# Optimization experiments

Measured on AMD Instinct MI355X. Metric: run time of the kernel, lower is better.

The kernel has to match this reference:

```python
import jax, jax.numpy as jnp
import numpy as np

SLOPE = 25.0  # fast_sigmoid surrogate slope
THR = 1.0     # snntorch Leaky default threshold

@jax.custom_vjp
def spike(x):
    # heaviside forward, fast-sigmoid surrogate backward
    return (x > 0).astype(x.dtype)

def _spike_fwd(x):
    return spike(x), x

def _spike_bwd(x, g):
    return (g / (SLOPE * jnp.abs(x) + 1.0) ** 2,)

spike.defvjp(_spike_fwd, _spike_bwd)


def _xavier(k, shape):
    fan_out, fan_in = shape
    lim = np.sqrt(6.0 / (fan_in + fan_out)).astype(np.float32)
    return jax.random.uniform(k, shape, jnp.float32, -lim, lim)


def setup_inputs() -> dict:
    key = jax.random.key(0)
    ks = jax.random.split(key, 6)
    B, T, NI, H1, H2, NO = 256, 100, 512, 1024, 1024, 10
    return {
        "x": jax.random.normal(ks[0], (B, T, NI), jnp.float32),
        "W1": _xavier(ks[1], (H1, NI)),
        "W1r": _xavier(ks[2], (H1, H1)),
        "W2": _xavier(ks[3], (H2, H1)),
        "W2r": _xavier(ks[4], (H2, H2)),
        "Wout": _xavier(ks[5], (NO, H2)),
        "beta1": jnp.float32(0.9),
        "beta2": jnp.float32(0.9),
        "beta_out": jnp.float32(0.9),
    }


def reference(x, W1, W1r, W2, W2r, Wout, beta1, beta2, beta_out):
    B, T, NI = x.shape
    H1, H2, NO = W1.shape[0], W2.shape[0], Wout.shape[0]
    b1 = jnp.clip(beta1, 0.0, 1.0)
    b2 = jnp.clip(beta2, 0.0, 1.0)
    bo = jnp.clip(beta_out, 0.0, 1.0)
    xt = jnp.transpose(x, (1, 0, 2))  # [T, B, NI]

    def step(carry, x_t):
        mem1, spk1, mem2, spk2, mem_out = carry
        # layer 1: feedforward + recurrent current, leaky integrate, subtract-reset
        cur1 = x_t @ W1.T + spk1 @ W1r.T
        reset1 = jax.lax.stop_gradient((mem1 > THR).astype(mem1.dtype))
        mem1 = b1 * mem1 + cur1 - reset1 * THR
        spk1 = spike(mem1 - THR)
        # layer 2
        cur2 = spk1 @ W2.T + spk2 @ W2r.T
        reset2 = jax.lax.stop_gradient((mem2 > THR).astype(mem2.dtype))
        mem2 = b2 * mem2 + cur2 - reset2 * THR
        spk2 = spike(mem2 - THR)
        # readout: reset_mechanism='none'
        mem_out = bo * mem_out + spk2 @ Wout.T
        return (mem1, spk1, mem2, spk2, mem_out), (spk1, mem_out)

    z = lambda n: jnp.zeros((B, n), x.dtype)
    carry0 = (z(H1), z(H1), z(H2), z(H2), z(NO))
    _, (spk1_rec, mem_out_rec) = jax.lax.scan(step, carry0, xt)
    return spk1_rec, mem_out_rec  # [T,B,H1], [T,B,NO]
```

## Files before the change

### kernel.cpp

```cpp
#include <hip/hip_runtime.h>

#define S_ELE (256 * 1024)
#define NBLK 1024
#define GRP  8
#define GSZ  (NBLK / GRP)

typedef float f32x4 __attribute__((ext_vector_type(4)));
typedef float f32x2 __attribute__((ext_vector_type(2)));

struct Ptrs {
    const float *x, *W1, *W1r, *W2, *W2r, *Wout;
    const float *b1, *b2, *bo;
    float *spk1_rec, *mout_rec;
    float *mem1, *mem2, *memo;
    float *w1rt, *w2t, *w2rt, *xw, *S2;
    unsigned *bar, *cnt1, *cnt2;
    unsigned short *idx1, *idx2;
    int t_ch;
};

__device__ __forceinline__ float clip01(float b) { return fminf(fmaxf(b, 0.0f), 1.0f); }
__device__ __forceinline__ float4 ld4(const float* p) { return *reinterpret_cast<const float4*>(p); }
__device__ __forceinline__ void   st4(float* p, float4 v) { *reinterpret_cast<float4*>(p) = v; }
__device__ __forceinline__ float2 ld2(const float* p) { return *reinterpret_cast<const float2*>(p); }
__device__ __forceinline__ void   st2(float* p, float2 v) { *reinterpret_cast<float2*>(p) = v; }
__device__ __forceinline__ void   st2nt(float* p, float2 v)
{
    f32x2 n = { v.x, v.y };
    __builtin_nontemporal_store(n, reinterpret_cast<f32x2*>(p));
}

__device__ __forceinline__ float4 memup(float4 mo, float4 cur, float b, float4* sv)
{
    float4 mn, s;
    mn.x = b * mo.x + cur.x - (mo.x > 1.0f ? 1.0f : 0.0f); s.x = (mn.x - 1.0f) > 0.0f ? 1.0f : 0.0f;
    mn.y = b * mo.y + cur.y - (mo.y > 1.0f ? 1.0f : 0.0f); s.y = (mn.y - 1.0f) > 0.0f ? 1.0f : 0.0f;
    mn.z = b * mo.z + cur.z - (mo.z > 1.0f ? 1.0f : 0.0f); s.z = (mn.z - 1.0f) > 0.0f ? 1.0f : 0.0f;
    mn.w = b * mo.w + cur.w - (mo.w > 1.0f ? 1.0f : 0.0f); s.w = (mn.w - 1.0f) > 0.0f ? 1.0f : 0.0f;
    *sv = s; return mn;
}
__device__ __forceinline__ float2 memup2(float2 mo, float2 cur, float b, float2* sv)
{
    float2 mn, s;
    mn.x = b * mo.x + cur.x - (mo.x > 1.0f ? 1.0f : 0.0f); s.x = (mn.x - 1.0f) > 0.0f ? 1.0f : 0.0f;
    mn.y = b * mo.y + cur.y - (mo.y > 1.0f ? 1.0f : 0.0f); s.y = (mn.y - 1.0f) > 0.0f ? 1.0f : 0.0f;
    *sv = s; return mn;
}

__device__ __forceinline__ void gbar(unsigned* bar)
{
    __syncthreads();
    if (threadIdx.x == 0) {
        unsigned g = __hip_atomic_load(&bar[0], __ATOMIC_RELAXED, __HIP_MEMORY_SCOPE_AGENT);
        unsigned* gc = &bar[8 + ((int)blockIdx.x & (GRP - 1)) * 32];
        unsigned a = __hip_atomic_fetch_add(gc, 1u, __ATOMIC_ACQ_REL, __HIP_MEMORY_SCOPE_AGENT);
        if (a == GSZ - 1) {
            __hip_atomic_store(gc, 0u, __ATOMIC_RELAXED, __HIP_MEMORY_SCOPE_AGENT);
            unsigned tp = __hip_atomic_fetch_add(&bar[1], 1u, __ATOMIC_ACQ_REL, __HIP_MEMORY_SCOPE_AGENT);
            if (tp == GRP - 1) {
                __hip_atomic_store(&bar[1], 0u, __ATOMIC_RELAXED, __HIP_MEMORY_SCOPE_AGENT);
                __hip_atomic_store(&bar[0], g + 1u, __ATOMIC_RELEASE, __HIP_MEMORY_SCOPE_AGENT);
            }
        }
        while (__hip_atomic_load(&bar[0], __ATOMIC_ACQUIRE, __HIP_MEMORY_SCOPE_AGENT) == g)
            __builtin_amdgcn_s_sleep(2);
    }
    __syncthreads();
}

__device__ __forceinline__ void tr32(float* sm, const float* src, float* dst, int tr, int tc)
{
    const int t = (int)threadIdx.x;
    const int r = t >> 3, c4 = (t & 7) << 2;
    __syncthreads();
    float4 v = ld4(src + (size_t)(tr * 32 + r) * 1024 + tc * 32 + c4);
    sm[r * 33 + c4 + 0] = v.x; sm[r * 33 + c4 + 1] = v.y;
    sm[r * 33 + c4 + 2] = v.z; sm[r * 33 + c4 + 3] = v.w;
    __syncthreads();
    const int kk = t >> 3, nn4 = (t & 7) << 2;
    float4 o;
    o.x = sm[(nn4 + 0) * 33 + kk]; o.y = sm[(nn4 + 1) * 33 + kk];
    o.z = sm[(nn4 + 2) * 33 + kk]; o.w = sm[(nn4 + 3) * 33 + kk];
    st4(dst + (size_t)(tc * 32 + kk) * 1024 + tr * 32 + nn4, o);
}

__device__ __forceinline__ void xw_tile(float* sm, const float* xA, const float* W1,
                                        float* out, int tm, int tn)
{
    float* As = sm;
    float* Bs = sm + 1056;
    const int t = (int)threadIdx.x;
    const int ar = t >> 1;
    const int ak = (t & 1) << 2;
    const int r0 = (t >> 4) << 3;
    const int c0 = (t & 15) << 3;
    const float* Ab = xA + (size_t)(tm * 128) * 51200;
    const float* Bb = W1 + (size_t)(tn * 128) * 512;
    float4 pa = ld4(Ab + (size_t)ar * 51200 + ak);
    float4 pb = ld4(Bb + (size_t)ar * 512 + ak);
    float acc[8][8] = {};
    for (int c = 0; c < 64; ++c) {
        __syncthreads();
        As[(ak + 0) * 132 + ar] = pa.x; As[(ak + 1) * 132 + ar] = pa.y;
        As[(ak + 2) * 132 + ar] = pa.z; As[(ak + 3) * 132 + ar] = pa.w;
        Bs[(ak + 0) * 132 + ar] = pb.x; Bs[(ak + 1) * 132 + ar] = pb.y;
        Bs[(ak + 2) * 132 + ar] = pb.z; Bs[(ak + 3) * 132 + ar] = pb.w;
        __syncthreads();
        if (c + 1 < 64) {
            const int ko = (c + 1) * 8;
            pa = ld4(Ab + (size_t)ar * 51200 + ko + ak);
            pb = ld4(Bb + (size_t)ar * 512 + ko + ak);
        }
        #pragma unroll
        for (int k = 0; k < 8; ++k) {
            float4 a0 = ld4(&As[k * 132 + r0]);
            float4 a1 = ld4(&As[k * 132 + r0 + 4]);
            float4 b0 = ld4(&Bs[k * 132 + c0]);
            float4 b1 = ld4(&Bs[k * 132 + c0 + 4]);
            float av[8] = {a0.x, a0.y, a0.z, a0.w, a1.x, a1.y, a1.z, a1.w};
            float bv[8] = {b0.x, b0.y, b0.z, b0.w, b1.x, b1.y, b1.z, b1.w};
            #pragma unroll
            for (int i = 0; i < 8; ++i)
                #pragma unroll
                for (int j = 0; j < 8; ++j)
                    acc[i][j] = fmaf(av[i], bv[j], acc[i][j]);
        }
    }
    #pragma unroll
    for (int i = 0; i < 8; ++i) {
        float* row = out + (size_t)(tm * 128 + r0 + i) * 1024 + tn * 128 + c0;
        st4(row,     make_float4(acc[i][0], acc[i][1], acc[i][2], acc[i][3]));
        st4(row + 4, make_float4(acc[i][4], acc[i][5], acc[i][6], acc[i][7]));
    }
}

template <int NC>
__device__ __forceinline__ void gatherN(const unsigned short* const lp[],
    const unsigned st[], const unsigned en[], const float* Wt, int n4, float4 c[])
{
    unsigned j[NC], e[NC];
    float4 pa[NC], pb[NC];
    #pragma unroll
    for (int q = 0; q < NC; ++q) {
        j[q] = st[q]; e[q] = en[q];
        c[q] = make_float4(0.f, 0.f, 0.f, 0.f);
        if (j[q] < e[q])     pa[q] = ld4(Wt + (size_t)lp[q][j[q]] * 1024 + n4);
        if (j[q] + 1 < e[q]) pb[q] = ld4(Wt + (size_t)lp[q][j[q] + 1] * 1024 + n4);
    }
    for (;;) {
        bool any = false;
        #pragma unroll
        for (int q = 0; q < NC; ++q) {
            if (j[q] < e[q]) {
                float4 v = pa[q];
                pa[q] = pb[q];
                if (j[q] + 2 < e[q]) pb[q] = ld4(Wt + (size_t)lp[q][j[q] + 2] * 1024 + n4);
                c[q].x += v.x; c[q].y += v.y; c[q].z += v.z; c[q].w += v.w;
                ++j[q];
                any = any || (j[q] < e[q]);
            }
        }
        if (!any) break;
    }
}

__device__ __forceinline__ void gather8_2(const unsigned short* lst,
    const unsigned pos[9], const float* Wt, int col, float2 c[8])
{
    unsigned j[8], e[8];
    float2 pa[8], pb[8];
    #pragma unroll
    for (int q = 0; q < 8; ++q) {
        j[q] = pos[q]; e[q] = pos[q + 1];
        c[q] = make_float2(0.f, 0.f);
        if (j[q] < e[q])     pa[q] = ld2(Wt + (size_t)lst[j[q]] * 1024 + col);
        if (j[q] + 1 < e[q]) pb[q] = ld2(Wt + (size_t)lst[j[q] + 1] * 1024 + col);
    }
    for (;;) {
        bool any = false;
        #pragma unroll
        for (int q = 0; q < 8; ++q) {
            if (j[q] < e[q]) {
                float2 v = pa[q];
                pa[q] = pb[q];
                if (j[q] + 2 < e[q]) pb[q] = ld2(Wt + (size_t)lst[j[q] + 2] * 1024 + col);
                c[q].x += v.x; c[q].y += v.y;
                ++j[q];
                any = any || (j[q] < e[q]);
            }
        }
        if (!any) break;
    }
}

__device__ __forceinline__ void build_seg_full(const float* s_spk,
    unsigned short* gidx, unsigned* gcnt)
{
    const int l = (int)threadIdx.x;
    #pragma unroll
    for (int w = 0; w < 8; ++w) {
        unsigned wtot = 0;
        #pragma unroll
        for (int i = 0; i < 2; ++i) {
            const int grp = w * 2 + i;
            float s = s_spk[grp * 64 + l];
            unsigned long long m = __ballot(s != 0.0f);
            unsigned off = (unsigned)__popcll(m & ((1ull << l) - 1ull));
            if (s != 0.0f) gidx[w * 128 + wtot + off] = (unsigned short)(grp * 64 + l);
            wtot += (unsigned)__popcll(m);
        }
        if (l == 0) gcnt[w] = wtot;
    }
}

__device__ __forceinline__ void build_seg_half(const float* s_half, int h,
    unsigned short* gidx, unsigned* gcnt)
{
    const int l = (int)threadIdx.x;
    #pragma unroll
    for (int wl = 0; wl < 4; ++wl) {
        const int w = 4 * h + wl;
        unsigned wtot = 0;
        #pragma unroll
        for (int i = 0; i < 2; ++i) {
            const int grp = wl * 2 + i;
            float s = s_half[grp * 64 + l];
            unsigned long long m = __ballot(s != 0.0f);
            unsigned off = (unsigned)__popcll(m & ((1ull << l) - 1ull));
            if (s != 0.0f)
                gidx[w * 128 + wtot + off] = (unsigned short)(h * 512 + grp * 64 + l);
            wtot += (unsigned)__popcll(m);
        }
        if (l == 0) gcnt[w] = wtot;
    }
}

__device__ __forceinline__ void stage_list(unsigned short* sl,
    const unsigned short* gseg, const unsigned* cw, const unsigned pos[9])
{
    const int t = (int)threadIdx.x;
    #pragma unroll
    for (int w = 0; w < 8; ++w)
        for (unsigned i = t; i < cw[w]; i += 256)
            sl[pos[w] + i] = gseg[w * 128 + i];
}

__device__ __forceinline__ void l1_half(float* sm, const Ptrs& p, int r, int h, int tau)
{
    const int t = (int)threadIdx.x;
    const int lc = t * 2;
    const int col = h * 512 + lc;
    const int pp = 1 - (tau & 1);
    const unsigned* cw = p.cnt1 + ((size_t)pp * 256 + r) * 8;
    unsigned pos[9];
    pos[0] = 0;
    #pragma unroll
    for (int w = 0; w < 8; ++w) pos[w + 1] = pos[w] + cw[w];
    unsigned short* sl16 = (unsigned short*)(sm + 512);
    stage_list(sl16, p.idx1 + ((size_t)pp * 256 + r) * 1024, cw, pos);
    __syncthreads();

    float2 c[8];
    gather8_2(sl16, pos, p.w1rt, col, c);

    const size_t base = (size_t)r * 1024 + col;
    const int slot = tau % p.t_ch;
    float2 acc = ld2(p.xw + (size_t)slot * S_ELE + base);
    #pragma unroll
    for (int w = 0; w < 8; ++w) { acc.x += c[w].x; acc.y += c[w].y; }
    const float bb = clip01(*p.b1);
    float2 mo = ld2(p.mem1 + base);
    float2 sv; float2 mn = memup2(mo, acc, bb, &sv);
    st2(p.mem1 + base, mn);
    st2nt(p.spk1_rec + (size_t)tau * S_ELE + base, sv);
    sm[lc] = sv.x; sm[lc + 1] = sv.y;
    __syncthreads();
    if (t < 64) build_seg_half(sm, h, p.idx1 + ((size_t)(tau & 1) * 256 + r) * 1024,
                               p.cnt1 + ((size_t)(tau & 1) * 256 + r) * 8);
}

__device__ __forceinline__ void l2g2(float* sm, const Ptrs& p, int g, int fam, int step)
{
    const int t = (int)threadIdx.x, n4 = t << 2;
    const bool rsel = fam >= 2;
    const bool hi = fam & 1;
    const int par = rsel ? (1 - (step & 1)) : (step & 1);
    const unsigned* cbase = (rsel ? p.cnt2 : p.cnt1) + (size_t)par * 256 * 8;
    const unsigned short* ibase = (rsel ? p.idx2 : p.idx1) + (size_t)par * 256 * 1024;
    const float* W = rsel ? p.w2rt : p.w2t;

    const unsigned short* lp[2];
    unsigned st[2], en[2];
    #pragma unroll
    for (int q = 0; q < 2; ++q) {
        const int r = 2 * g + q;
        const unsigned* cw = cbase + (size_t)r * 8;
        unsigned pos[9];
        pos[0] = 0;
        #pragma unroll
        for (int w = 0; w < 8; ++w) pos[w + 1] = pos[w] + cw[w];
        unsigned short* sl = (unsigned short*)sm + 1024 * q;
        stage_list(sl, ibase + (size_t)r * 1024, cw, pos);
        lp[q] = sl;
        st[q] = hi ? pos[4] : 0;
        en[q] = hi ? pos[8] : pos[4];
    }
    __syncthreads();
    float4 c[2];
    gatherN<2>(lp, st, en, W, n4, c);
    #pragma unroll
    for (int q = 0; q < 2; ++q)
        st4(p.S2 + (size_t)fam * S_ELE + (size_t)(2 * g + q) * 1024 + n4, c[q]);
}

__device__ __forceinline__ void upd2_row(float* sm, const Ptrs& p, int r, int step)
{
    const int t = (int)threadIdx.x, n4 = t << 2;
    const size_t base = (size_t)r * 1024 + n4;
    float4 p0 = ld4(p.S2 + base);
    float4 p1 = ld4(p.S2 + (size_t)S_ELE + base);
    float4 p2 = ld4(p.S2 + (size_t)2 * S_ELE + base);
    float4 p3 = ld4(p.S2 + (size_t)3 * S_ELE + base);
    float4 cur;
    cur.x = (p0.x + p1.x) + (p2.x + p3.x);
    cur.y = (p0.y + p1.y) + (p2.y + p3.y);
    cur.z = (p0.z + p1.z) + (p2.z + p3.z);
    cur.w = (p0.w + p1.w) + (p2.w + p3.w);
    const float bb = clip01(*p.b2);
    float4 mo = ld4(p.mem2 + base);
    float4 sv; float4 mn = memup(mo, cur, bb, &sv);
    st4(p.mem2 + base, mn);
    sm[n4 + 0] = sv.x; sm[n4 + 1] = sv.y; sm[n4 + 2] = sv.z; sm[n4 + 3] = sv.w;
    __syncthreads();
    if (t < 64) build_seg_full(sm, p.idx2 + ((size_t)(step & 1) * 256 + r) * 1024,
                               p.cnt2 + ((size_t)(step & 1) * 256 + r) * 8);
    const int wave = t >> 6, lane = t & 63;
    const float bo = clip01(*p.bo);
    float v[16];
    #pragma unroll
    for (int i = 0; i < 16; ++i) v[i] = sm[lane + 64 * i];
    float* rec = p.mout_rec + (size_t)step * 2560;
    for (int o = wave; o < 10; o += 4) {
        float sum = 0.0f;
        #pragma unroll
        for (int i = 0; i < 16; ++i)
            sum = fmaf(v[i], p.Wout[o * 1024 + lane + 64 * i], sum);
        #pragma unroll
        for (int off = 32; off > 0; off >>= 1) sum += __shfl_down(sum, off);
        if (lane == 0) {
            const float m = bo * p.memo[r * 10 + o] + sum;
            p.memo[r * 10 + o] = m;
            __builtin_nontemporal_store(m, &rec[r * 10 + o]);
        }
    }
}

__global__ __launch_bounds__(256, 4) void snn_all(Ptrs p)
{
    __shared__ float sm[2176];
    const int bid = (int)blockIdx.x;
    const int x = bid & 7, g = bid >> 3;

    for (int task = bid; task < 3072; task += NBLK) {
        const float* src = task < 1024 ? p.W1r : (task < 2048 ? p.W2 : p.W2r);
        float* dst = task < 1024 ? p.w1rt : (task < 2048 ? p.w2t : p.w2rt);
        const int id = task & 1023;
        tr32(sm, src, dst, id >> 5, id & 31);
    }
    gbar(p.bar);

    for (int tau = 0; tau <= 100; ++tau) {
        if (tau < 100 && (tau % p.t_ch) == 0) {
            const int ntask = p.t_ch * 16;
            for (int task = bid; task < ntask; task += NBLK) {
                const int tp = task >> 4, tile = task & 15;
                xw_tile(sm, p.x + (size_t)(tau + tp) * 512, p.W1,
                        p.xw + (size_t)tp * S_ELE, tile >> 3, tile & 7);
            }
            gbar(p.bar);
        }
        if (x < 4) {
            if (tau < 100) {
                const int idx = x * 128 + g;
                l1_half(sm, p, idx >> 1, idx & 1, tau);
            }
        } else {
            if (tau >= 1) l2g2(sm, p, g, x - 4, tau - 1);
        }
        gbar(p.bar);
        if (bid < 256 && tau >= 1) upd2_row(sm, p, bid, tau - 1);
        gbar(p.bar);
    }
}

__global__ __launch_bounds__(256, 4) void fb_pre(Ptrs p)
{
    __shared__ float sm[2176];
    for (int task = blockIdx.x; task < 3072; task += gridDim.x) {
        const float* src = task < 1024 ? p.W1r : (task < 2048 ? p.W2 : p.W2r);
        float* dst = task < 1024 ? p.w1rt : (task < 2048 ? p.w2t : p.w2rt);
        const int id = task & 1023;
        tr32(sm, src, dst, id >> 5, id & 31);
    }
}

__global__ __launch_bounds__(256, 4) void fb_xw(Ptrs p, int t0)
{
    __shared__ float sm[2176];
    const int task = (int)blockIdx.x;
    const int tp = task >> 4, tile = task & 15;
    xw_tile(sm, p.x + (size_t)(t0 + tp) * 512, p.W1,
            p.xw + (size_t)tp * S_ELE, tile >> 3, tile & 7);
}

__global__ __launch_bounds__(256, 4) void fb_p1(Ptrs p, int tau)
{
    __shared__ float sm[2176];
    const int bid = (int)blockIdx.x;
    const int x = bid & 7, g = bid >> 3;
    if (x < 4) {
        if (tau < 100) {
            const int idx = x * 128 + g;
            l1_half(sm, p, idx >> 1, idx & 1, tau);
        }
    } else {
        if (tau >= 1) l2g2(sm, p, g, x - 4, tau - 1);
    }
}

__global__ __launch_bounds__(256, 4) void fb_p2(Ptrs p, int tau)
{
    __shared__ float sm[2176];
    if (tau >= 1) upd2_row(sm, p, (int)blockIdx.x, tau - 1);
}

extern "C" void kernel_launch(void* const* d_in, const int* in_sizes, int n_in,
                              void* d_out, int out_size, void* d_ws, size_t ws_size,
                              hipStream_t stream)
{
    Ptrs p;
    p.x    = (const float*)d_in[0];
    p.W1   = (const float*)d_in[1];
    p.W1r  = (const float*)d_in[2];
    p.W2   = (const float*)d_in[3];
    p.W2r  = (const float*)d_in[4];
    p.Wout = (const float*)d_in[5];
    p.b1   = (const float*)d_in[6];
    p.b2   = (const float*)d_in[7];
    p.bo   = (const float*)d_in[8];

    float* out = (float*)d_out;
    p.spk1_rec = out;
    p.mout_rec = out + (size_t)100 * S_ELE;

    float* w = (float*)d_ws;
    p.mem1 = w;  w += S_ELE;
    p.mem2 = w;  w += S_ELE;
    p.memo = w;  w += 2560;
    p.bar  = (unsigned*)w;  w += 512;
    p.cnt1 = (unsigned*)w;  w += 4096;
    p.cnt2 = (unsigned*)w;  w += 4096;
    p.idx1 = (unsigned short*)w;  w += 262144;
    p.idx2 = (unsigned short*)w;  w += 262144;
    p.w1rt = w;  w += 1048576;
    p.w2t  = w;  w += 1048576;
    p.w2rt = w;  w += 1048576;
    p.S2   = w;  w += 4 * S_ELE;
    p.xw   = w;

    const size_t used = (size_t)(w - (float*)d_ws) * sizeof(float);
    int t_ch = 1;
    const int cands[] = {100, 50, 25, 20, 10, 5, 4, 2, 1};
    for (int c : cands)
        if (used + (size_t)c * S_ELE * sizeof(float) <= ws_size) { t_ch = c; break; }
    p.t_ch = t_ch;

    (void)hipMemsetAsync(p.mem1, 0,
                   ((size_t)2 * S_ELE + 2560 + 512 + 8192) * sizeof(float), stream);

    int maxb = 0;
    hipError_t qerr = hipOccupancyMaxActiveBlocksPerMultiprocessor(
        &maxb, (const void*)snn_all, 256, 0);
    bool coop = (qerr == hipSuccess && maxb >= 4);

    if (coop) {
        void* args[] = { (void*)&p };
        if (hipLaunchCooperativeKernel((const void*)snn_all, dim3(NBLK), dim3(256),
                                       args, 0, stream) != hipSuccess)
            coop = false;
    }

    if (!coop) {
        hipLaunchKernelGGL(fb_pre, dim3(NBLK), dim3(256), 0, stream, p);
        for (int tau = 0; tau <= 100; ++tau) {
            if (tau < 100 && (tau % t_ch) == 0)
                hipLaunchKernelGGL(fb_xw, dim3(t_ch * 16), dim3(256), 0, stream, p, tau);
            hipLaunchKernelGGL(fb_p1, dim3(NBLK), dim3(256), 0, stream, p, tau);
            hipLaunchKernelGGL(fb_p2, dim3(256), dim3(256), 0, stream, p, tau);
        }
    }
}
```

Before: 4.024 ms.

## Double the persistent grid to 2048 blocks with finer per-block work

Doubles the cooperative grid from 1024 to 2048 blocks at 8 blocks per CU. Each layer-1 block now handles a quarter row with one column per thread instead of half a row with two. Each layer-2 gather block now handles one row instead of two. Shared memory is halved and the xw tile loop uses 4-wide k chunks so more blocks fit per CU, aiming to hide gather latency through occupancy. The cost is more participants in every grid barrier, scalar rather than vector loads in the gathers, and a cooperative launch that now needs an occupancy of 8 to run.

After: 13.17 ms. 227% more time.

```diff
diff --git a/kernel.cpp b/kernel.cpp
--- a/kernel.cpp
+++ b/kernel.cpp
@@ -1,12 +1,11 @@
 #include <hip/hip_runtime.h>
 
 #define S_ELE (256 * 1024)
-#define NBLK 1024
+#define NBLK 2048
 #define GRP  8
 #define GSZ  (NBLK / GRP)
 
 typedef float f32x4 __attribute__((ext_vector_type(4)));
-typedef float f32x2 __attribute__((ext_vector_type(2)));
 
 struct Ptrs {
     const float *x, *W1, *W1r, *W2, *W2r, *Wout;
@@ -22,13 +21,6 @@
 __device__ __forceinline__ float clip01(float b) { return fminf(fmaxf(b, 0.0f), 1.0f); }
 __device__ __forceinline__ float4 ld4(const float* p) { return *reinterpret_cast<const float4*>(p); }
 __device__ __forceinline__ void   st4(float* p, float4 v) { *reinterpret_cast<float4*>(p) = v; }
-__device__ __forceinline__ float2 ld2(const float* p) { return *reinterpret_cast<const float2*>(p); }
-__device__ __forceinline__ void   st2(float* p, float2 v) { *reinterpret_cast<float2*>(p) = v; }
-__device__ __forceinline__ void   st2nt(float* p, float2 v)
-{
-    f32x2 n = { v.x, v.y };
-    __builtin_nontemporal_store(n, reinterpret_cast<f32x2*>(p));
-}
 
 __device__ __forceinline__ float4 memup(float4 mo, float4 cur, float b, float4* sv)
 {
@@ -39,12 +31,11 @@
     mn.w = b * mo.w + cur.w - (mo.w > 1.0f ? 1.0f : 0.0f); s.w = (mn.w - 1.0f) > 0.0f ? 1.0f : 0.0f;
     *sv = s; return mn;
 }
-__device__ __forceinline__ float2 memup2(float2 mo, float2 cur, float b, float2* sv)
-{
-    float2 mn, s;
-    mn.x = b * mo.x + cur.x - (mo.x > 1.0f ? 1.0f : 0.0f); s.x = (mn.x - 1.0f) > 0.0f ? 1.0f : 0.0f;
-    mn.y = b * mo.y + cur.y - (mo.y > 1.0f ? 1.0f : 0.0f); s.y = (mn.y - 1.0f) > 0.0f ? 1.0f : 0.0f;
-    *sv = s; return mn;
+__device__ __forceinline__ float memup1(float mo, float cur, float b, float* sv)
+{
+    float mn = b * mo + cur - (mo > 1.0f ? 1.0f : 0.0f);
+    *sv = (mn - 1.0f) > 0.0f ? 1.0f : 0.0f;
+    return mn;
 }
 
 __device__ __forceinline__ void gbar(unsigned* bar)
@@ -88,31 +79,27 @@
                                         float* out, int tm, int tn)
 {
     float* As = sm;
-    float* Bs = sm + 1056;
+    float* Bs = sm + 528;
     const int t = (int)threadIdx.x;
-    const int ar = t >> 1;
-    const int ak = (t & 1) << 2;
+    const int half = t >> 7;
+    const int row  = t & 127;
     const int r0 = (t >> 4) << 3;
     const int c0 = (t & 15) << 3;
     const float* Ab = xA + (size_t)(tm * 128) * 51200;
     const float* Bb = W1 + (size_t)(tn * 128) * 512;
-    float4 pa = ld4(Ab + (size_t)ar * 51200 + ak);
-    float4 pb = ld4(Bb + (size_t)ar * 512 + ak);
+    const float* src = half ? (Bb + (size_t)row * 512) : (Ab + (size_t)row * 51200);
+    float* dstbase = half ? Bs : As;
+
+    float4 pv = ld4(src);
     float acc[8][8] = {};
-    for (int c = 0; c < 64; ++c) {
+    for (int c = 0; c < 128; ++c) {
         __syncthreads();
-        As[(ak + 0) * 132 + ar] = pa.x; As[(ak + 1) * 132 + ar] = pa.y;
-        As[(ak + 2) * 132 + ar] = pa.z; As[(ak + 3) * 132 + ar] = pa.w;
-        Bs[(ak + 0) * 132 + ar] = pb.x; Bs[(ak + 1) * 132 + ar] = pb.y;
-        Bs[(ak + 2) * 132 + ar] = pb.z; Bs[(ak + 3) * 132 + ar] = pb.w;
+        dstbase[0 * 132 + row] = pv.x; dstbase[1 * 132 + row] = pv.y;
+        dstbase[2 * 132 + row] = pv.z; dstbase[3 * 132 + row] = pv.w;
         __syncthreads();
-        if (c + 1 < 64) {
-            const int ko = (c + 1) * 8;
-            pa = ld4(Ab + (size_t)ar * 51200 + ko + ak);
-            pb = ld4(Bb + (size_t)ar * 512 + ko + ak);
-        }
-        #pragma unroll
-        for (int k = 0; k < 8; ++k) {
+        if (c + 1 < 128) pv = ld4(src + (c + 1) * 4);
+        #pragma unroll
+        for (int k = 0; k < 4; ++k) {
             float4 a0 = ld4(&As[k * 132 + r0]);
             float4 a1 = ld4(&As[k * 132 + r0 + 4]);
             float4 b0 = ld4(&Bs[k * 132 + c0]);
@@ -128,63 +115,50 @@
     }
     #pragma unroll
     for (int i = 0; i < 8; ++i) {
-        float* row = out + (size_t)(tm * 128 + r0 + i) * 1024 + tn * 128 + c0;
-        st4(row,     make_float4(acc[i][0], acc[i][1], acc[i][2], acc[i][3]));
-        st4(row + 4, make_float4(acc[i][4], acc[i][5], acc[i][6], acc[i][7]));
-    }
-}
-
-template <int NC>
-__device__ __forceinline__ void gatherN(const unsigned short* const lp[],
-    const unsigned st[], const unsigned en[], const float* Wt, int n4, float4 c[])
-{
-    unsigned j[NC], e[NC];
-    float4 pa[NC], pb[NC];
-    #pragma unroll
-    for (int q = 0; q < NC; ++q) {
-        j[q] = st[q]; e[q] = en[q];
-        c[q] = make_float4(0.f, 0.f, 0.f, 0.f);
-        if (j[q] < e[q])     pa[q] = ld4(Wt + (size_t)lp[q][j[q]] * 1024 + n4);
-        if (j[q] + 1 < e[q]) pb[q] = ld4(Wt + (size_t)lp[q][j[q] + 1] * 1024 + n4);
+        float* rowp = out + (size_t)(tm * 128 + r0 + i) * 1024 + tn * 128 + c0;
+        st4(rowp,     make_float4(acc[i][0], acc[i][1], acc[i][2], acc[i][3]));
+        st4(rowp + 4, make_float4(acc[i][4], acc[i][5], acc[i][6], acc[i][7]));
+    }
+}
+
+__device__ __forceinline__ float4 gather1_4(const unsigned short* lst,
+    unsigned j, unsigned e, const float* Wt, int n4)
+{
+    float4 c = make_float4(0.f, 0.f, 0.f, 0.f);
+    float4 pa, pb;
+    if (j < e)     pa = ld4(Wt + (size_t)lst[j] * 1024 + n4);
+    if (j + 1 < e) pb = ld4(Wt + (size_t)lst[j + 1] * 1024 + n4);
+    while (j < e) {
+        float4 v = pa;
+        pa = pb;
+        if (j + 2 < e) pb = ld4(Wt + (size_t)lst[j + 2] * 1024 + n4);
+        c.x += v.x; c.y += v.y; c.z += v.z; c.w += v.w;
+        ++j;
+    }
+    return c;
+}
+
+__device__ __forceinline__ void gather8_1(const unsigned short* lst,
+    const unsigned pos[9], const float* Wt, int col, float c[8])
+{
+    unsigned j[8], e[8];
+    float pa[8], pb[8];
+    #pragma unroll
+    for (int q = 0; q < 8; ++q) {
+        j[q] = pos[q]; e[q] = pos[q + 1];
+        c[q] = 0.0f;
+        if (j[q] < e[q])     pa[q] = Wt[(size_t)lst[j[q]] * 1024 + col];
+        if (j[q] + 1 < e[q]) pb[q] = Wt[(size_t)lst[j[q] + 1] * 1024 + col];
     }
     for (;;) {
         bool any = false;
         #pragma unroll
-        for (int q = 0; q < NC; ++q) {
-            if (j[q] < e[q]) {
-                float4 v = pa[q];
-                pa[q] = pb[q];
-                if (j[q] + 2 < e[q]) pb[q] = ld4(Wt + (size_t)lp[q][j[q] + 2] * 1024 + n4);
-                c[q].x += v.x; c[q].y += v.y; c[q].z += v.z; c[q].w += v.w;
-                ++j[q];
-                any = any || (j[q] < e[q]);
-            }
-        }
-        if (!any) break;
-    }
-}
-
-__device__ __forceinline__ void gather8_2(const unsigned short* lst,
-    const unsigned pos[9], const float* Wt, int col, float2 c[8])
-{
-    unsigned j[8], e[8];
-    float2 pa[8], pb[8];
-    #pragma unroll
-    for (int q = 0; q < 8; ++q) {
-        j[q] = pos[q]; e[q] = pos[q + 1];
-        c[q] = make_float2(0.f, 0.f);
-        if (j[q] < e[q])     pa[q] = ld2(Wt + (size_t)lst[j[q]] * 1024 + col);
-        if (j[q] + 1 < e[q]) pb[q] = ld2(Wt + (size_t)lst[j[q] + 1] * 1024 + col);
-    }
-    for (;;) {
-        bool any = false;
-        #pragma unroll
         for (int q = 0; q < 8; ++q) {
             if (j[q] < e[q]) {
-                float2 v = pa[q];
+                float v = pa[q];
                 pa[q] = pb[q];
-                if (j[q] + 2 < e[q]) pb[q] = ld2(Wt + (size_t)lst[j[q] + 2] * 1024 + col);
-                c[q].x += v.x; c[q].y += v.y;
+                if (j[q] + 2 < e[q]) pb[q] = Wt[(size_t)lst[j[q] + 2] * 1024 + col];
+                c[q] += v;
                 ++j[q];
                 any = any || (j[q] < e[q]);
             }
@@ -213,22 +187,22 @@
     }
 }
 
-__device__ __forceinline__ void build_seg_half(const float* s_half, int h,
+__device__ __forceinline__ void build_seg_quarter(const float* s_q, int q,
     unsigned short* gidx, unsigned* gcnt)
 {
     const int l = (int)threadIdx.x;
     #pragma unroll
-    for (int wl = 0; wl < 4; ++wl) {
-        const int w = 4 * h + wl;
+    for (int wl = 0; wl < 2; ++wl) {
+        const int w = 2 * q + wl;
         unsigned wtot = 0;
         #pragma unroll
         for (int i = 0; i < 2; ++i) {
             const int grp = wl * 2 + i;
-            float s = s_half[grp * 64 + l];
+            float s = s_q[grp * 64 + l];
             unsigned long long m = __ballot(s != 0.0f);
             unsigned off = (unsigned)__popcll(m & ((1ull << l) - 1ull));
             if (s != 0.0f)
-                gidx[w * 128 + wtot + off] = (unsigned short)(h * 512 + grp * 64 + l);
+                gidx[w * 128 + wtot + off] = (unsigned short)(q * 256 + grp * 64 + l);
             wtot += (unsigned)__popcll(m);
         }
         if (l == 0) gcnt[w] = wtot;
@@ -245,72 +219,61 @@
             sl[pos[w] + i] = gseg[w * 128 + i];
 }
 
-__device__ __forceinline__ void l1_half(float* sm, const Ptrs& p, int r, int h, int tau)
+__device__ __forceinline__ void l1_quarter(float* sm, const Ptrs& p, int r, int q, int tau)
 {
     const int t = (int)threadIdx.x;
-    const int lc = t * 2;
-    const int col = h * 512 + lc;
+    const int col = q * 256 + t;
     const int pp = 1 - (tau & 1);
     const unsigned* cw = p.cnt1 + ((size_t)pp * 256 + r) * 8;
     unsigned pos[9];
     pos[0] = 0;
     #pragma unroll
     for (int w = 0; w < 8; ++w) pos[w + 1] = pos[w] + cw[w];
-    unsigned short* sl16 = (unsigned short*)(sm + 512);
+    unsigned short* sl16 = (unsigned short*)(sm + 256);
     stage_list(sl16, p.idx1 + ((size_t)pp * 256 + r) * 1024, cw, pos);
     __syncthreads();
 
-    float2 c[8];
-    gather8_2(sl16, pos, p.w1rt, col, c);
+    float c[8];
+    gather8_1(sl16, pos, p.w1rt, col, c);
 
     const size_t base = (size_t)r * 1024 + col;
     const int slot = tau % p.t_ch;
-    float2 acc = ld2(p.xw + (size_t)slot * S_ELE + base);
-    #pragma unroll
-    for (int w = 0; w < 8; ++w) { acc.x += c[w].x; acc.y += c[w].y; }
+    float acc = p.xw[(size_t)slot * S_ELE + base];
+    #pragma unroll
+    for (int w = 0; w < 8; ++w) acc += c[w];
     const float bb = clip01(*p.b1);
-    float2 mo = ld2(p.mem1 + base);
-    float2 sv; float2 mn = memup2(mo, acc, bb, &sv);
-    st2(p.mem1 + base, mn);
-    st2nt(p.spk1_rec + (size_t)tau * S_ELE + base, sv);
-    sm[lc] = sv.x; sm[lc + 1] = sv.y;
-    __syncthreads();
-    if (t < 64) build_seg_half(sm, h, p.idx1 + ((size_t)(tau & 1) * 256 + r) * 1024,
-                               p.cnt1 + ((size_t)(tau & 1) * 256 + r) * 8);
-}
-
-__device__ __forceinline__ void l2g2(float* sm, const Ptrs& p, int g, int fam, int step)
+    float sv;
+    float mn = memup1(p.mem1[base], acc, bb, &sv);
+    p.mem1[base] = mn;
+    __builtin_nontemporal_store(sv, &p.spk1_rec[(size_t)tau * S_ELE + base]);
+    sm[t] = sv;
+    __syncthreads();
+    if (t < 64) build_seg_quarter(sm, q, p.idx1 + ((size_t)(tau & 1) * 256 + r) * 1024,
+                                  p.cnt1 + ((size_t)(tau & 1) * 256 + r) * 8);
+}
+
+__device__ __forceinline__ void l2g1(float* sm, const Ptrs& p, int r, int fam, int step)
 {
     const int t = (int)threadIdx.x, n4 = t << 2;
     const bool rsel = fam >= 2;
     const bool hi = fam & 1;
     const int par = rsel ? (1 - (step & 1)) : (step & 1);
-    const unsigned* cbase = (rsel ? p.cnt2 : p.cnt1) + (size_t)par * 256 * 8;
-    const unsigned short* ibase = (rsel ? p.idx2 : p.idx1) + (size_t)par * 256 * 1024;
+    const unsigned* cw = ((rsel ? p.cnt2 : p.cnt1) + (size_t)par * 256 * 8) + (size_t)r * 8;
+    const unsigned short* gseg = ((rsel ? p.idx2 : p.idx1) + (size_t)par * 256 * 1024)
+                                 + (size_t)r * 1024;
     const float* W = rsel ? p.w2rt : p.w2t;
 
-    const unsigned short* lp[2];
-    unsigned st[2], en[2];
-    #pragma unroll
-    for (int q = 0; q < 2; ++q) {
-        const int r = 2 * g + q;
-        const unsigned* cw = cbase + (size_t)r * 8;
-        unsigned pos[9];
-        pos[0] = 0;
-        #pragma unroll
-        for (int w = 0; w < 8; ++w) pos[w + 1] = pos[w] + cw[w];
-        unsigned short* sl = (unsigned short*)sm + 1024 * q;
-        stage_list(sl, ibase + (size_t)r * 1024, cw, pos);
-        lp[q] = sl;
-        st[q] = hi ? pos[4] : 0;
-        en[q] = hi ? pos[8] : pos[4];
-    }
-    __syncthreads();
-    float4 c[2];
-    gatherN<2>(lp, st, en, W, n4, c);
-    #pragma unroll
-    for (int q = 0; q < 2; ++q)
-        st4(p.S2 + (size_t)fam * S_ELE + (size_t)(2 * g + q) * 1024 + n4, c[q]);
+    unsigned pos[9];
+    pos[0] = 0;
+    #pragma unroll
+    for (int w = 0; w < 8; ++w) pos[w + 1] = pos[w] + cw[w];
+    unsigned short* sl = (unsigned short*)sm;
+    stage_list(sl, gseg, cw, pos);
+    __syncthreads();
+    const unsigned st = hi ? pos[4] : 0;
+    const unsigned en = hi ? pos[8] : pos[4];
+    float4 c = gather1_4(sl, st, en, W, n4);
+    st4(p.S2 + (size_t)fam * S_ELE + (size_t)r * 1024 + n4, c);
 }
 
 __device__ __forceinline__ void upd2_row(float* sm, const Ptrs& p, int r, int step)
@@ -355,9 +318,9 @@
     }
 }
 
-__global__ __launch_bounds__(256, 4) void snn_all(Ptrs p)
-{
-    __shared__ float sm[2176];
+__global__ __launch_bounds__(256, 8) void snn_all(Ptrs p)
+{
+    __shared__ float sm[1088];
     const int bid = (int)blockIdx.x;
     const int x = bid & 7, g = bid >> 3;
 
@@ -380,12 +343,9 @@
             gbar(p.bar);
         }
         if (x < 4) {
-            if (tau < 100) {
-                const int idx = x * 128 + g;
-                l1_half(sm, p, idx >> 1, idx & 1, tau);
-            }
+            if (tau < 100) l1_quarter(sm, p, g, x, tau);
         } else {
-            if (tau >= 1) l2g2(sm, p, g, x - 4, tau - 1);
+            if (tau >= 1) l2g1(sm, p, g, x - 4, tau - 1);
         }
         gbar(p.bar);
         if (bid < 256 && tau >= 1) upd2_row(sm, p, bid, tau - 1);
@@ -393,9 +353,9 @@
     }
 }
 
-__global__ __launch_bounds__(256, 4) void fb_pre(Ptrs p)
-{
-    __shared__ float sm[2176];
+__global__ __launch_bounds__(256, 8) void fb_pre(Ptrs p)
+{
+    __shared__ float sm[1088];
     for (int task = blockIdx.x; task < 3072; task += gridDim.x) {
         const float* src = task < 1024 ? p.W1r : (task < 2048 ? p.W2 : p.W2r);
         float* dst = task < 1024 ? p.w1rt : (task < 2048 ? p.w2t : p.w2rt);
@@ -404,33 +364,30 @@
     }
 }
 
-__global__ __launch_bounds__(256, 4) void fb_xw(Ptrs p, int t0)
-{
-    __shared__ float sm[2176];
+__global__ __launch_bounds__(256, 8) void fb_xw(Ptrs p, int t0)
+{
+    __shared__ float sm[1088];
     const int task = (int)blockIdx.x;
     const int tp = task >> 4, tile = task & 15;
     xw_tile(sm, p.x + (size_t)(t0 + tp) * 512, p.W1,
             p.xw + (size_t)tp * S_ELE, tile >> 3, tile & 7);
 }
 
-__global__ __launch_bounds__(256, 4) void fb_p1(Ptrs p, int tau)
-{
-    __shared__ float sm[2176];
+__global__ __launch_bounds__(256, 8) void fb_p1(Ptrs p, int tau)
+{
+    __shared__ float sm[1088];
     const int bid = (int)blockIdx.x;
     const int x = bid & 7, g = bid >> 3;
     if (x < 4) {
-        if (tau < 100) {
-            const int idx = x * 128 + g;
-            l1_half(sm, p, idx >> 1, idx & 1, tau);
-        }
+        if (tau < 100) l1_quarter(sm, p, g, x, tau);
     } else {
-        if (tau >= 1) l2g2(sm, p, g, x - 4, tau - 1);
-    }
-}
-
-__global__ __launch_bounds__(256, 4) void fb_p2(Ptrs p, int tau)
-{
-    __shared__ float sm[2176];
+        if (tau >= 1) l2g1(sm, p, g, x - 4, tau - 1);
+    }
+}
+
+__global__ __launch_bounds__(256, 8) void fb_p2(Ptrs p, int tau)
+{
+    __shared__ float sm[1088];
     if (tau >= 1) upd2_row(sm, p, (int)blockIdx.x, tau - 1);
 }
 
@@ -481,7 +438,7 @@
     int maxb = 0;
     hipError_t qerr = hipOccupancyMaxActiveBlocksPerMultiprocessor(
         &maxb, (const void*)snn_all, 256, 0);
-    bool coop = (qerr == hipSuccess && maxb >= 4);
+    bool coop = (qerr == hipSuccess && maxb >= 8);
 
     if (coop) {
         void* args[] = { (void*)&p };
```
